# Kernel optimization log

Hardware: AMD Instinct MI355X
Metric: run time of the kernel (lower is better)

The kernel has to match this reference:

```python
import jax, jax.numpy as jnp
import numpy as np

H = 16          # ATTENTION_HEAD
E = 300         # EXPANSION_LENGTH
D = 768         # TEXT_EMBEDDING_DIM
HD = D // H     # 48


def setup_inputs() -> dict:
    key = jax.random.key(0)
    ks = jax.random.split(key, 10)
    b, n, ql, kl = 1, 4, 64, 64
    q = jax.random.normal(ks[0], (b, n, ql, D), dtype=jnp.float32)
    k = jax.random.normal(ks[1], (b, 1, kl, D), dtype=jnp.float32)
    v = jax.random.normal(ks[2], (b, 1, kl, D), dtype=jnp.float32)
    s = 1.0 / np.sqrt(D)
    Wq = jax.random.normal(ks[3], (D, D), dtype=jnp.float32) * s
    bq = jnp.zeros((D,), dtype=jnp.float32)
    Wk = jax.random.normal(ks[4], (D, D), dtype=jnp.float32) * s
    bk = jnp.zeros((D,), dtype=jnp.float32)
    Wv = jax.random.normal(ks[5], (D, D), dtype=jnp.float32) * s
    bv = jnp.zeros((D,), dtype=jnp.float32)
    memory = jax.random.normal(ks[6], (1, E, H, HD), dtype=jnp.float32) * 0.05
    return {"q": q, "k": k, "v": v, "Wq": Wq, "bq": bq, "Wk": Wk,
            "bk": bk, "Wv": Wv, "bv": bv, "memory": memory}


def reference(q, k, v, Wq, bq, Wk, bk, Wv, bv, memory):
    b, n, ql, _ = q.shape
    kl = k.shape[2]
    # Dense projections
    Q = (q @ Wq + bq).reshape(b, n, ql, H, HD)          # bnqhd
    K = (k @ Wk + bk).reshape(b, kl, H, HD)             # bkhd
    V = (v @ Wv + bv).reshape(b, kl, H, HD)             # bkhd
    # memory (1,E,H,HD) -> (1,E,1,H,HD); K -> (b,1,kl,H,HD); broadcast sum
    broad_sum = memory[:, :, None, :, :] + K[:, None, :, :, :]   # bekhd
    M = jax.nn.relu(jnp.einsum('bekhd,bnqhd->bnekqh', broad_sum, Q))
    E_seq = jnp.einsum('bnekqh,bkhd->bnekhd', M, V)
    out = jnp.einsum('bnekhd,bnekqh->bnqhd', E_seq, M)
    return out.reshape(q.shape)
```

## Files before the change

### kernel.cpp

```cpp
#include <hip/hip_runtime.h>

#define H   16
#define E   300
#define D   768
#define HD  48
#define QL  64
#define KL  64
#define NH  64
#define ROWS 384
#define SPLITK 12
#define NCH 16

#define OFF_PP 0
#define OFF_PF (SPLITK*ROWS*D)
#define OFF_A  (OFF_PF + ROWS*D)
#define OFF_B  (OFF_A + NH*E*QL)
#define OFF_SP (OFF_B + NH*KL*QL)

__global__ __launch_bounds__(256, 1) void proj_kernel(
    const float* __restrict__ qin, const float* __restrict__ kin, const float* __restrict__ vin,
    const float* __restrict__ Wq, const float* __restrict__ Wk, const float* __restrict__ Wv,
    float* __restrict__ ws)
{
    const int rowblk = blockIdx.x;
    const int col0   = blockIdx.y * 128;
    const int ks     = blockIdx.z;
    const int kbase  = ks * 64;

    const int g0 = rowblk * 128;
    const float* Wlo = (g0      < 256) ? Wq : (g0      < 320) ? Wk : Wv;
    const float* Whi = (g0 + 64 < 256) ? Wq : (g0 + 64 < 320) ? Wk : Wv;

    __shared__ float XsT[32][132];
    __shared__ float Ws2[2][32][128];

    const int tid = threadIdx.x;
    const int r0  = (tid >> 4) * 8;
    const int c0  = (tid & 15) * 8;
    const int hw  = r0 >> 6;

    float acc[8][8];
    #pragma unroll
    for (int i = 0; i < 8; i++)
        #pragma unroll
        for (int j = 0; j < 8; j++) acc[i][j] = 0.f;

    for (int kk2 = 0; kk2 < 64; kk2 += 32) {
        #pragma unroll
        for (int it = 0; it < 4; it++) {
            const int idx = it * 256 + tid;
            const int row = idx >> 3;
            const int d4  = (idx & 7) * 4;
            const int grow = rowblk * 128 + row;
            const float* src = (grow < 256) ? (qin + grow * D)
                             : (grow < 320) ? (kin + (grow - 256) * D)
                                            : (vin + (grow - 320) * D);
            const float4 xv = *(const float4*)(src + kbase + kk2 + d4);
            XsT[d4 + 0][row] = xv.x; XsT[d4 + 1][row] = xv.y;
            XsT[d4 + 2][row] = xv.z; XsT[d4 + 3][row] = xv.w;
        }
        #pragma unroll
        for (int it = 0; it < 8; it++) {
            const int idx  = it * 256 + tid;
            const int half = idx >> 10;
            const int rem  = idx & 1023;
            const int dk   = rem >> 5;
            const int c4   = (rem & 31) * 4;
            const float* Wsel = half ? Whi : Wlo;
            *(float4*)&Ws2[half][dk][c4] =
                *(const float4*)(Wsel + (kbase + kk2 + dk) * D + col0 + c4);
        }
        __syncthreads();
        #pragma unroll
        for (int dk = 0; dk < 32; dk++) {
            const float4 x0 = *(const float4*)&XsT[dk][r0];
            const float4 x1 = *(const float4*)&XsT[dk][r0 + 4];
            const float4 w0 = *(const float4*)&Ws2[hw][dk][c0];
            const float4 w1 = *(const float4*)&Ws2[hw][dk][c0 + 4];
            const float xr[8] = {x0.x, x0.y, x0.z, x0.w, x1.x, x1.y, x1.z, x1.w};
            const float wc[8] = {w0.x, w0.y, w0.z, w0.w, w1.x, w1.y, w1.z, w1.w};
            #pragma unroll
            for (int i = 0; i < 8; i++)
                #pragma unroll
                for (int j = 0; j < 8; j++)
                    acc[i][j] = fmaf(xr[i], wc[j], acc[i][j]);
        }
        __syncthreads();
    }
    float* P = ws + OFF_PP + ks * (ROWS * D);
    #pragma unroll
    for (int i = 0; i < 8; i++) {
        float* base = P + (rowblk * 128 + r0 + i) * D + col0 + c0;
        *(float4*)(base)     = make_float4(acc[i][0], acc[i][1], acc[i][2], acc[i][3]);
        *(float4*)(base + 4) = make_float4(acc[i][4], acc[i][5], acc[i][6], acc[i][7]);
    }
}

__global__ __launch_bounds__(256) void reduce_kernel(
    const float* __restrict__ bq, const float* __restrict__ bk, const float* __restrict__ bv,
    float* __restrict__ ws)
{
    const int idx = (blockIdx.x * 256 + threadIdx.x) * 4;
    const float* PP = ws + OFF_PP;
    float4 v = *(const float4*)(PP + idx);
    #pragma unroll
    for (int c = 1; c < SPLITK; c++) {
        const float4 p = *(const float4*)(PP + c * (ROWS * D) + idx);
        v.x += p.x; v.y += p.y; v.z += p.z; v.w += p.w;
    }
    const int row = idx / D, col = idx % D;
    const float* bias = (row < 256) ? bq : (row < 320) ? bk : bv;
    const float4 b = *(const float4*)(bias + col);
    v.x += b.x; v.y += b.y; v.z += b.z; v.w += b.w;
    *(float4*)(ws + OFF_PF + idx) = v;
}

__global__ __launch_bounds__(256) void ab_kernel(
    const float* __restrict__ memo, float* __restrict__ ws)
{
    const int nh = blockIdx.x;
    const int rg = blockIdx.y;
    const int n = nh >> 4, h = nh & 15;
    const float* Pf = ws + OFF_PF;
    float* A = ws + OFF_A;
    float* B = ws + OFF_B;

    __shared__ float RsT[48][132];
    __shared__ float QsT[48][68];

    const int tid = threadIdx.x;
    #pragma unroll
    for (int it = 0; it < 6; it++) {
        const int idx = it * 256 + tid;
        const int row = idx / 12;
        const int d4  = (idx % 12) * 4;
        const int rr = rg * 128 + row;
        float4 rv = make_float4(0.f, 0.f, 0.f, 0.f);
        if (rr < E)            rv = *(const float4*)(memo + rr * D + h * HD + d4);
        else if (rr < E + KL)  rv = *(const float4*)(Pf + (256 + rr - E) * D + h * HD + d4);
        RsT[d4 + 0][row] = rv.x; RsT[d4 + 1][row] = rv.y;
        RsT[d4 + 2][row] = rv.z; RsT[d4 + 3][row] = rv.w;
    }
    #pragma unroll
    for (int it = 0; it < 3; it++) {
        const int idx = it * 256 + tid;
        const int q  = idx / 12;
        const int d4 = (idx % 12) * 4;
        const float4 qv = *(const float4*)(Pf + (n * QL + q) * D + h * HD + d4);
        QsT[d4 + 0][q] = qv.x; QsT[d4 + 1][q] = qv.y;
        QsT[d4 + 2][q] = qv.z; QsT[d4 + 3][q] = qv.w;
    }
    __syncthreads();

    const int r0 = (tid >> 4) * 8;
    const int q0 = (tid & 15) * 4;
    float acc[8][4];
    #pragma unroll
    for (int i = 0; i < 8; i++)
        #pragma unroll
        for (int j = 0; j < 4; j++) acc[i][j] = 0.f;

    #pragma unroll 4
    for (int d = 0; d < HD; d++) {
        const float4 rf0 = *(const float4*)&RsT[d][r0];
        const float4 rf1 = *(const float4*)&RsT[d][r0 + 4];
        const float4 qf  = *(const float4*)&QsT[d][q0];
        const float rr8[8] = {rf0.x, rf0.y, rf0.z, rf0.w, rf1.x, rf1.y, rf1.z, rf1.w};
        const float qq4[4] = {qf.x, qf.y, qf.z, qf.w};
        #pragma unroll
        for (int i = 0; i < 8; i++)
            #pragma unroll
            for (int j = 0; j < 4; j++)
                acc[i][j] = fmaf(rr8[i], qq4[j], acc[i][j]);
    }
    #pragma unroll
    for (int i = 0; i < 8; i++) {
        const int rr = rg * 128 + r0 + i;
        const float4 av = make_float4(acc[i][0], acc[i][1], acc[i][2], acc[i][3]);
        if (rr < E)            *(float4*)(A + (nh * E + rr) * QL + q0) = av;
        else if (rr < E + KL)  *(float4*)(B + (nh * KL + (rr - E)) * QL + q0) = av;
    }
}

__global__ __launch_bounds__(256, 1) void main_kernel(float* __restrict__ ws)
{
    const int nh = blockIdx.x;
    const int cg = blockIdx.y;
    const int tid = threadIdx.x;
    const int lane = tid & 63;
    const int w = tid >> 6;

    __shared__ float As[75 * 64];
    __shared__ float Bs[64][68];

    const float* Ag = ws + OFF_A + (nh * E + cg * 75) * QL;
    for (int idx = tid; idx < 1200; idx += 256)
        *(float4*)&As[idx * 4] = *(const float4*)(Ag + idx * 4);
    const float* Bg = ws + OFF_B + nh * (KL * QL);
    #pragma unroll
    for (int it = 0; it < 4; it++) {
        const int idx = it * 256 + tid;
        const int k  = idx >> 4;
        const int q4 = (idx & 15) * 4;
        *(float4*)&Bs[k][q4] = *(const float4*)(Bg + idx * 4);
    }
    __syncthreads();

    float b[64];
    #pragma unroll
    for (int j = 0; j < 16; j++)
        *(float4*)&b[j * 4] = *(const float4*)&Bs[lane][j * 4];

    float s[64];
    #pragma unroll
    for (int j = 0; j < 64; j++) s[j] = 0.f;

    const int eBeg = w * 19;
    const int eEnd = (eBeg + 19 < 75) ? eBeg + 19 : 75;
    for (int e = eBeg; e < eEnd; e++) {
        float m[64];
        #pragma unroll
        for (int j4 = 0; j4 < 16; j4++) {
            const float4 a = *(const float4*)&As[e * 64 + j4 * 4];
            m[j4 * 4 + 0] = fmaxf(a.x + b[j4 * 4 + 0], 0.f);
            m[j4 * 4 + 1] = fmaxf(a.y + b[j4 * 4 + 1], 0.f);
            m[j4 * 4 + 2] = fmaxf(a.z + b[j4 * 4 + 2], 0.f);
            m[j4 * 4 + 3] = fmaxf(a.w + b[j4 * 4 + 3], 0.f);
        }
        float p0 = 0.f, p1 = 0.f, p2 = 0.f, p3 = 0.f;
        #pragma unroll
        for (int j4 = 0; j4 < 16; j4++) {
            p0 += m[j4 * 4 + 0]; p1 += m[j4 * 4 + 1];
            p2 += m[j4 * 4 + 2]; p3 += m[j4 * 4 + 3];
        }
        const float p = (p0 + p1) + (p2 + p3);
        #pragma unroll
        for (int j = 0; j < 64; j++)
            s[j] = fmaf(m[j], p, s[j]);
    }

    float* Sp = ws + OFF_SP + (((cg * 4 + w) * NH + nh) * QL) * KL;
    #pragma unroll
    for (int q = 0; q < 64; q++)
        Sp[q * KL + lane] = s[q];
}

__global__ __launch_bounds__(256) void out_kernel(
    const float* __restrict__ ws_c, float* __restrict__ outp)
{
    const int nh = blockIdx.x;
    const int qq = blockIdx.y;
    const int n = nh >> 4, h = nh & 15;
    const int q0 = qq * 16;
    const float* Sp = ws_c + OFF_SP;
    const float* Pf = ws_c + OFF_PF;

    __shared__ float S_l[16][64];
    __shared__ float V_l[64][52];

    const int tid = threadIdx.x;
    #pragma unroll
    for (int it = 0; it < 4; it++) {
        const int idx = it * 256 + tid;
        const int qi = idx >> 6, k = idx & 63;
        float sum = 0.f;
        #pragma unroll
        for (int c = 0; c < NCH; c++)
            sum += Sp[((c * NH + nh) * QL + q0 + qi) * KL + k];
        S_l[qi][k] = sum;
    }
    #pragma unroll
    for (int it = 0; it < 3; it++) {
        const int idx = it * 256 + tid;
        const int k  = idx / 12;
        const int d4 = (idx % 12) * 4;
        *(float4*)&V_l[k][d4] = *(const float4*)(Pf + (320 + k) * D + h * HD + d4);
    }
    __syncthreads();

    const int qi = tid >> 4;
    const int dg = tid & 15;
    if (dg < 12) {
        float a0 = 0.f, a1 = 0.f, a2 = 0.f, a3 = 0.f;
        #pragma unroll 8
        for (int k = 0; k < KL; k++) {
            const float sv = S_l[qi][k];
            const float4 vf = *(const float4*)&V_l[k][dg * 4];
            a0 = fmaf(sv, vf.x, a0); a1 = fmaf(sv, vf.y, a1);
            a2 = fmaf(sv, vf.z, a2); a3 = fmaf(sv, vf.w, a3);
        }
        *(float4*)(outp + (n * QL + q0 + qi) * D + h * HD + dg * 4) =
            make_float4(a0, a1, a2, a3);
    }
}

extern "C" void kernel_launch(void* const* d_in, const int* in_sizes, int n_in,
                              void* d_out, int out_size, void* d_ws, size_t ws_size,
                              hipStream_t stream)
{
    const float* q    = (const float*)d_in[0];
    const float* k    = (const float*)d_in[1];
    const float* v    = (const float*)d_in[2];
    const float* Wq   = (const float*)d_in[3];
    const float* bq   = (const float*)d_in[4];
    const float* Wk   = (const float*)d_in[5];
    const float* bk   = (const float*)d_in[6];
    const float* Wv   = (const float*)d_in[7];
    const float* bv   = (const float*)d_in[8];
    const float* memo = (const float*)d_in[9];
    float* ws   = (float*)d_ws;
    float* outp = (float*)d_out;

    hipLaunchKernelGGL(proj_kernel, dim3(3, 6, 12), dim3(256), 0, stream,
                       q, k, v, Wq, Wk, Wv, ws);
    hipLaunchKernelGGL(reduce_kernel, dim3(288), dim3(256), 0, stream, bq, bk, bv, ws);
    hipLaunchKernelGGL(ab_kernel, dim3(64, 3), dim3(256), 0, stream, memo, ws);
    hipLaunchKernelGGL(main_kernel, dim3(64, 4), dim3(256), 0, stream, ws);
    hipLaunchKernelGGL(out_kernel, dim3(64, 4), dim3(256), 0, stream, ws, outp);
}
```

Before: 124.5 us.

## Fuse split-K reduction and bias into consumer kernels, drop reduce kernel

Removes the separate reduce kernel. The ab_kernel and out_kernel now sum the 12 split-K partials and add the bias directly when loading Q, K and V tiles. This saves one kernel launch and the round trip through a finalized projection buffer, but the partials are re-read redundantly: Q/K by the three rg blocks, V by the four q blocks. The projection kernel's thread-to-tile mapping is also rearranged so each half of the block handles one 64-row half, with strided 4x4 sub-tiles.

```diff
diff --git a/kernel.cpp b/kernel.cpp
--- a/kernel.cpp
+++ b/kernel.cpp
@@ -9,11 +9,10 @@
 #define NH  64
 #define ROWS 384
 #define SPLITK 12
-#define NCH 16
+#define NCHUNK 16
 
 #define OFF_PP 0
-#define OFF_PF (SPLITK*ROWS*D)
-#define OFF_A  (OFF_PF + ROWS*D)
+#define OFF_A  (SPLITK*ROWS*D)
 #define OFF_B  (OFF_A + NH*E*QL)
 #define OFF_SP (OFF_B + NH*KL*QL)
 
@@ -26,18 +25,18 @@
     const int col0   = blockIdx.y * 128;
     const int ks     = blockIdx.z;
     const int kbase  = ks * 64;
-
-    const int g0 = rowblk * 128;
-    const float* Wlo = (g0      < 256) ? Wq : (g0      < 320) ? Wk : Wv;
-    const float* Whi = (g0 + 64 < 256) ? Wq : (g0 + 64 < 320) ? Wk : Wv;
+    const int g0     = rowblk * 128;
+    const float* Wlo = (g0      < 256) ? Wq : Wk;
+    const float* Whi = (g0 + 64 < 256) ? Wq : Wv;
 
     __shared__ float XsT[32][132];
     __shared__ float Ws2[2][32][128];
 
-    const int tid = threadIdx.x;
-    const int r0  = (tid >> 4) * 8;
-    const int c0  = (tid & 15) * 8;
-    const int hw  = r0 >> 6;
+    const int tid  = threadIdx.x;
+    const int half = tid >> 7;
+    const int loc  = tid & 127;
+    const int r0a  = (loc >> 4) * 4;
+    const int c0a  = (loc & 15) * 4;
 
     float acc[8][8];
     #pragma unroll
@@ -51,7 +50,7 @@
             const int idx = it * 256 + tid;
             const int row = idx >> 3;
             const int d4  = (idx & 7) * 4;
-            const int grow = rowblk * 128 + row;
+            const int grow = g0 + row;
             const float* src = (grow < 256) ? (qin + grow * D)
                              : (grow < 320) ? (kin + (grow - 256) * D)
                                             : (vin + (grow - 320) * D);
@@ -61,24 +60,23 @@
         }
         #pragma unroll
         for (int it = 0; it < 8; it++) {
-            const int idx  = it * 256 + tid;
-            const int half = idx >> 10;
-            const int rem  = idx & 1023;
-            const int dk   = rem >> 5;
-            const int c4   = (rem & 31) * 4;
-            const float* Wsel = half ? Whi : Wlo;
-            *(float4*)&Ws2[half][dk][c4] =
-                *(const float4*)(Wsel + (kbase + kk2 + dk) * D + col0 + c4);
+            const int idx = it * 256 + tid;
+            const int s   = idx >> 10;
+            const int rem = idx & 1023;
+            const int dk  = rem >> 5;
+            const int c4  = (rem & 31) * 4;
+            *(float4*)&Ws2[s][dk][c4] =
+                *(const float4*)((s ? Whi : Wlo) + (kbase + kk2 + dk) * D + col0 + c4);
         }
         __syncthreads();
         #pragma unroll
         for (int dk = 0; dk < 32; dk++) {
-            const float4 x0 = *(const float4*)&XsT[dk][r0];
-            const float4 x1 = *(const float4*)&XsT[dk][r0 + 4];
-            const float4 w0 = *(const float4*)&Ws2[hw][dk][c0];
-            const float4 w1 = *(const float4*)&Ws2[hw][dk][c0 + 4];
-            const float xr[8] = {x0.x, x0.y, x0.z, x0.w, x1.x, x1.y, x1.z, x1.w};
-            const float wc[8] = {w0.x, w0.y, w0.z, w0.w, w1.x, w1.y, w1.z, w1.w};
+            const float4 xa = *(const float4*)&XsT[dk][half * 64 + r0a];
+            const float4 xb = *(const float4*)&XsT[dk][half * 64 + r0a + 32];
+            const float4 wa = *(const float4*)&Ws2[half][dk][c0a];
+            const float4 wb = *(const float4*)&Ws2[half][dk][c0a + 64];
+            const float xr[8] = {xa.x, xa.y, xa.z, xa.w, xb.x, xb.y, xb.z, xb.w};
+            const float wc[8] = {wa.x, wa.y, wa.z, wa.w, wb.x, wb.y, wb.z, wb.w};
             #pragma unroll
             for (int i = 0; i < 8; i++)
                 #pragma unroll
@@ -90,65 +88,61 @@
     float* P = ws + OFF_PP + ks * (ROWS * D);
     #pragma unroll
     for (int i = 0; i < 8; i++) {
-        float* base = P + (rowblk * 128 + r0 + i) * D + col0 + c0;
-        *(float4*)(base)     = make_float4(acc[i][0], acc[i][1], acc[i][2], acc[i][3]);
-        *(float4*)(base + 4) = make_float4(acc[i][4], acc[i][5], acc[i][6], acc[i][7]);
-    }
-}
-
-__global__ __launch_bounds__(256) void reduce_kernel(
-    const float* __restrict__ bq, const float* __restrict__ bk, const float* __restrict__ bv,
+        const int row = g0 + half * 64 + r0a + (i < 4 ? i : 28 + i);
+        *(float4*)(P + row * D + col0 + c0a) =
+            make_float4(acc[i][0], acc[i][1], acc[i][2], acc[i][3]);
+        *(float4*)(P + row * D + col0 + c0a + 64) =
+            make_float4(acc[i][4], acc[i][5], acc[i][6], acc[i][7]);
+    }
+}
+
+__global__ __launch_bounds__(256, 1) void ab_kernel(
+    const float* __restrict__ memo,
+    const float* __restrict__ bq_, const float* __restrict__ bk_,
     float* __restrict__ ws)
-{
-    const int idx = (blockIdx.x * 256 + threadIdx.x) * 4;
-    const float* PP = ws + OFF_PP;
-    float4 v = *(const float4*)(PP + idx);
-    #pragma unroll
-    for (int c = 1; c < SPLITK; c++) {
-        const float4 p = *(const float4*)(PP + c * (ROWS * D) + idx);
-        v.x += p.x; v.y += p.y; v.z += p.z; v.w += p.w;
-    }
-    const int row = idx / D, col = idx % D;
-    const float* bias = (row < 256) ? bq : (row < 320) ? bk : bv;
-    const float4 b = *(const float4*)(bias + col);
-    v.x += b.x; v.y += b.y; v.z += b.z; v.w += b.w;
-    *(float4*)(ws + OFF_PF + idx) = v;
-}
-
-__global__ __launch_bounds__(256) void ab_kernel(
-    const float* __restrict__ memo, float* __restrict__ ws)
 {
     const int nh = blockIdx.x;
     const int rg = blockIdx.y;
     const int n = nh >> 4, h = nh & 15;
-    const float* Pf = ws + OFF_PF;
+    const float* PP = ws + OFF_PP;
     float* A = ws + OFF_A;
     float* B = ws + OFF_B;
 
+    __shared__ float QsT[48][68];
     __shared__ float RsT[48][132];
-    __shared__ float QsT[48][68];
 
     const int tid = threadIdx.x;
-    #pragma unroll
-    for (int it = 0; it < 6; it++) {
-        const int idx = it * 256 + tid;
-        const int row = idx / 12;
-        const int d4  = (idx % 12) * 4;
-        const int rr = rg * 128 + row;
-        float4 rv = make_float4(0.f, 0.f, 0.f, 0.f);
-        if (rr < E)            rv = *(const float4*)(memo + rr * D + h * HD + d4);
-        else if (rr < E + KL)  rv = *(const float4*)(Pf + (256 + rr - E) * D + h * HD + d4);
-        RsT[d4 + 0][row] = rv.x; RsT[d4 + 1][row] = rv.y;
-        RsT[d4 + 2][row] = rv.z; RsT[d4 + 3][row] = rv.w;
-    }
-    #pragma unroll
-    for (int it = 0; it < 3; it++) {
-        const int idx = it * 256 + tid;
-        const int q  = idx / 12;
-        const int d4 = (idx % 12) * 4;
-        const float4 qv = *(const float4*)(Pf + (n * QL + q) * D + h * HD + d4);
-        QsT[d4 + 0][q] = qv.x; QsT[d4 + 1][q] = qv.y;
-        QsT[d4 + 2][q] = qv.z; QsT[d4 + 3][q] = qv.w;
+    for (int l = tid; l < 64 * 12; l += 256) {
+        const int q  = l / 12;
+        const int d4 = (l % 12) * 4;
+        float4 s = make_float4(0.f, 0.f, 0.f, 0.f);
+        #pragma unroll
+        for (int c = 0; c < SPLITK; c++) {
+            const float4 p = *(const float4*)(PP + c * (ROWS * D) + (n * QL + q) * D + h * HD + d4);
+            s.x += p.x; s.y += p.y; s.z += p.z; s.w += p.w;
+        }
+        const float4 bb = *(const float4*)(bq_ + h * HD + d4);
+        QsT[d4 + 0][q] = s.x + bb.x; QsT[d4 + 1][q] = s.y + bb.y;
+        QsT[d4 + 2][q] = s.z + bb.z; QsT[d4 + 3][q] = s.w + bb.w;
+    }
+    for (int l = tid; l < 128 * 12; l += 256) {
+        const int row = l / 12;
+        const int d4  = (l % 12) * 4;
+        const int rr  = rg * 128 + row;
+        float4 s = make_float4(0.f, 0.f, 0.f, 0.f);
+        if (rr < E) {
+            s = *(const float4*)(memo + rr * D + h * HD + d4);
+        } else if (rr < E + KL) {
+            #pragma unroll
+            for (int c = 0; c < SPLITK; c++) {
+                const float4 p = *(const float4*)(PP + c * (ROWS * D) + (256 + rr - E) * D + h * HD + d4);
+                s.x += p.x; s.y += p.y; s.z += p.z; s.w += p.w;
+            }
+            const float4 bb = *(const float4*)(bk_ + h * HD + d4);
+            s.x += bb.x; s.y += bb.y; s.z += bb.z; s.w += bb.w;
+        }
+        RsT[d4 + 0][row] = s.x; RsT[d4 + 1][row] = s.y;
+        RsT[d4 + 2][row] = s.z; RsT[d4 + 3][row] = s.w;
     }
     __syncthreads();
 
@@ -166,12 +160,13 @@
         const float4 rf1 = *(const float4*)&RsT[d][r0 + 4];
         const float4 qf  = *(const float4*)&QsT[d][q0];
         const float rr8[8] = {rf0.x, rf0.y, rf0.z, rf0.w, rf1.x, rf1.y, rf1.z, rf1.w};
-        const float qq4[4] = {qf.x, qf.y, qf.z, qf.w};
-        #pragma unroll
-        for (int i = 0; i < 8; i++)
-            #pragma unroll
-            for (int j = 0; j < 4; j++)
-                acc[i][j] = fmaf(rr8[i], qq4[j], acc[i][j]);
+        #pragma unroll
+        for (int i = 0; i < 8; i++) {
+            acc[i][0] = fmaf(rr8[i], qf.x, acc[i][0]);
+            acc[i][1] = fmaf(rr8[i], qf.y, acc[i][1]);
+            acc[i][2] = fmaf(rr8[i], qf.z, acc[i][2]);
+            acc[i][3] = fmaf(rr8[i], qf.w, acc[i][3]);
+        }
     }
     #pragma unroll
     for (int i = 0; i < 8; i++) {
@@ -185,7 +180,7 @@
 __global__ __launch_bounds__(256, 1) void main_kernel(float* __restrict__ ws)
 {
     const int nh = blockIdx.x;
-    const int cg = blockIdx.y;
+    const int cgI = blockIdx.y;
     const int tid = threadIdx.x;
     const int lane = tid & 63;
     const int w = tid >> 6;
@@ -193,7 +188,7 @@
     __shared__ float As[75 * 64];
     __shared__ float Bs[64][68];
 
-    const float* Ag = ws + OFF_A + (nh * E + cg * 75) * QL;
+    const float* Ag = ws + OFF_A + (nh * E + cgI * 75) * QL;
     for (int idx = tid; idx < 1200; idx += 256)
         *(float4*)&As[idx * 4] = *(const float4*)(Ag + idx * 4);
     const float* Bg = ws + OFF_B + nh * (KL * QL);
@@ -239,42 +234,47 @@
             s[j] = fmaf(m[j], p, s[j]);
     }
 
-    float* Sp = ws + OFF_SP + (((cg * 4 + w) * NH + nh) * QL) * KL;
+    float* Sp = ws + OFF_SP + ((cgI * 4 + w) * NH + nh) * (QL * KL);
     #pragma unroll
     for (int q = 0; q < 64; q++)
         Sp[q * KL + lane] = s[q];
 }
 
-__global__ __launch_bounds__(256) void out_kernel(
-    const float* __restrict__ ws_c, float* __restrict__ outp)
+__global__ __launch_bounds__(256, 1) void out_kernel(
+    const float* __restrict__ ws_c, const float* __restrict__ bv_, float* __restrict__ outp)
 {
     const int nh = blockIdx.x;
     const int qq = blockIdx.y;
     const int n = nh >> 4, h = nh & 15;
     const int q0 = qq * 16;
     const float* Sp = ws_c + OFF_SP;
-    const float* Pf = ws_c + OFF_PF;
-
-    __shared__ float S_l[16][64];
+    const float* PP = ws_c + OFF_PP;
+
+    __shared__ float S_l[16][65];
     __shared__ float V_l[64][52];
 
     const int tid = threadIdx.x;
+    for (int l = tid; l < 64 * 12; l += 256) {
+        const int k  = l / 12;
+        const int d4 = (l % 12) * 4;
+        float4 s = make_float4(0.f, 0.f, 0.f, 0.f);
+        #pragma unroll
+        for (int c = 0; c < SPLITK; c++) {
+            const float4 p = *(const float4*)(PP + c * (ROWS * D) + (320 + k) * D + h * HD + d4);
+            s.x += p.x; s.y += p.y; s.z += p.z; s.w += p.w;
+        }
+        const float4 bb = *(const float4*)(bv_ + h * HD + d4);
+        *(float4*)&V_l[k][d4] = make_float4(s.x + bb.x, s.y + bb.y, s.z + bb.z, s.w + bb.w);
+    }
     #pragma unroll
     for (int it = 0; it < 4; it++) {
         const int idx = it * 256 + tid;
         const int qi = idx >> 6, k = idx & 63;
         float sum = 0.f;
         #pragma unroll
-        for (int c = 0; c < NCH; c++)
+        for (int c = 0; c < NCHUNK; c++)
             sum += Sp[((c * NH + nh) * QL + q0 + qi) * KL + k];
         S_l[qi][k] = sum;
-    }
-    #pragma unroll
-    for (int it = 0; it < 3; it++) {
-        const int idx = it * 256 + tid;
-        const int k  = idx / 12;
-        const int d4 = (idx % 12) * 4;
-        *(float4*)&V_l[k][d4] = *(const float4*)(Pf + (320 + k) * D + h * HD + d4);
     }
     __syncthreads();
 
@@ -313,8 +313,7 @@
 
     hipLaunchKernelGGL(proj_kernel, dim3(3, 6, 12), dim3(256), 0, stream,
                        q, k, v, Wq, Wk, Wv, ws);
-    hipLaunchKernelGGL(reduce_kernel, dim3(288), dim3(256), 0, stream, bq, bk, bv, ws);
-    hipLaunchKernelGGL(ab_kernel, dim3(64, 3), dim3(256), 0, stream, memo, ws);
+    hipLaunchKernelGGL(ab_kernel, dim3(64, 3), dim3(256), 0, stream, memo, bq, bk, ws);
     hipLaunchKernelGGL(main_kernel, dim3(64, 4), dim3(256), 0, stream, ws);
-    hipLaunchKernelGGL(out_kernel, dim3(64, 4), dim3(256), 0, stream, ws, outp);
-}
+    hipLaunchKernelGGL(out_kernel, dim3(64, 4), dim3(256), 0, stream, ws, bv, outp);
+}
```

Result: slower. 140.7 us (+13.0%).
